# Performance work log

Hardware: AMD Instinct MI355X
Metric: run time of the kernel (lower is better)

Reference implementation:

```python
import jax, jax.numpy as jnp
import numpy as np

B, S, D, H, L = 128, 256, 128, 4, 2
N = S - 1            # tree nodes (complete binary tree, depths 0..7)
MAX_DEPTH = 7
NEG = -1e9
EPS = 1e-6


def _binary_tree_topology():
    n = np.arange(N)
    parent = np.where(n > 0, (n - 1) // 2, 0).astype(np.int32)   # parent(0) dummy
    depth = np.floor(np.log2(n + 1)).astype(np.int32)            # BFS level
    is_leaf = (2 * n + 1 >= N)
    return parent, depth, is_leaf


def setup_inputs() -> dict:
    key = jax.random.key(0)
    ks = jax.random.split(key, 6)
    p_np, d_np, l_np = _binary_tree_topology()
    parent = jnp.broadcast_to(jnp.asarray(p_np), (B, N))
    depth = jnp.broadcast_to(jnp.asarray(d_np), (B, N))
    is_leaf = jnp.broadcast_to(jnp.asarray(l_np), (B, N))
    x = jax.random.normal(ks[0], (B, S, D), jnp.float32)
    mask = jnp.zeros((B, 1, 1, S), jnp.float32)  # full trees -> no padding
    sc = 1.0 / np.sqrt(D)
    Wq = jax.random.normal(ks[1], (L, D, D), jnp.float32) * sc
    Wk = jax.random.normal(ks[2], (L, D, D), jnp.float32) * sc
    Wv = jax.random.normal(ks[3], (L, D, D), jnp.float32) * sc
    Wo = jax.random.normal(ks[4], (L, D, D), jnp.float32) * sc
    bq = jnp.zeros((L, D)); bk = jnp.zeros((L, D)); bv = jnp.zeros((L, D)); bo = jnp.zeros((L, D))
    g1 = jnp.ones((L, D)); b1 = jnp.zeros((L, D))
    g2 = jnp.ones((L, D)); b2 = jnp.zeros((L, D))
    return dict(x=x, mask=mask, parent=parent, depth=depth, is_leaf=is_leaf,
                Wq=Wq, bq=bq, Wk=Wk, bk=bk, Wv=Wv, bv=bv, Wo=Wo, bo=bo,
                g1=g1, b1=b1, g2=g2, b2=b2)


def _layernorm(x, g, b):
    mu = jnp.mean(x, axis=-1, keepdims=True)
    var = jnp.mean(jnp.square(x - mu), axis=-1, keepdims=True)
    return g * (x - mu) * jax.lax.rsqrt(var + EPS) + b


def _tree_agg(x, parent, depth, is_leaf):
    """Vectorized bottom-up tree aggregation (agg='sum': tanh(sum children)).
    Seq positions map to tree nodes in BFS order; last position passes through."""
    e = x[:, :N]                                            # [B, N, D]
    seg = (parent + (jnp.arange(B) * N)[:, None]).reshape(-1)  # flat parent ids
    for d in range(MAX_DEPTH, 0, -1):                       # deepest level -> root
        contrib = jnp.where((depth == d)[..., None], e, 0.0)
        agg = jax.ops.segment_sum(contrib.reshape(B * N, D), seg,
                                  num_segments=B * N).reshape(B, N, D)
        upd = ((depth == d - 1) & (~is_leaf))[..., None]    # internal nodes at d-1
        e = jnp.where(upd, jnp.tanh(agg), e)
    return jnp.concatenate([e, x[:, N:]], axis=1)


def reference(x, mask, parent, depth, is_leaf,
              Wq, bq, Wk, bk, Wv, bv, Wo, bo, g1, b1, g2, b2):
    Dh = D // H
    scale = 1.0 / jnp.sqrt(jnp.float32(Dh))
    losses = []
    weights = None
    for l in range(L):
        q = (jnp.einsum('bsd,de->bse', x, Wq[l]) + bq[l]).reshape(B, S, H, Dh).transpose(0, 2, 1, 3)
        k = (jnp.einsum('bsd,de->bse', x, Wk[l]) + bk[l]).reshape(B, S, H, Dh).transpose(0, 2, 1, 3)
        v = (jnp.einsum('bsd,de->bse', x, Wv[l]) + bv[l]).reshape(B, S, H, Dh).transpose(0, 2, 1, 3)
        logits = jnp.einsum('bhqd,bhkd->bhqk', q, k) * scale + mask * NEG
        attn = jax.nn.softmax(logits, axis=-1)              # [B, H, S, S]
        ctx = jnp.einsum('bhqk,bhkd->bhqd', attn, v).transpose(0, 2, 1, 3).reshape(B, S, D)
        att_out = jnp.einsum('bsd,de->bse', ctx, Wo[l]) + bo[l]
        out1 = _layernorm(x + att_out, g1[l], b1[l])
        tab = _tree_agg(out1, parent, depth, is_leaf)       # dropout: eval -> identity
        x = _layernorm(out1 + tab, g2[l], b2[l])
        weights = attn[:, :, -1, :]
        losses.append(jnp.sum(jnp.abs(weights)))
    total_l1 = jnp.sum(jnp.stack(losses))
    return x, total_l1, weights
```

## Files before the change

kernel.cpp:

```cpp
#include <hip/hip_runtime.h>
#include <math.h>

typedef __bf16 bf16x8 __attribute__((ext_vector_type(8)));
typedef __bf16 bf16x2 __attribute__((ext_vector_type(2)));
typedef float f32x4 __attribute__((ext_vector_type(4)));

namespace {
constexpr int kB = 128, kS = 256, kD = 128, kH = 4;
constexpr float kEps = 1e-6f;
constexpr float kScale = 0.17677669529663687f;
constexpr float kNeg = -1000000000.0f;
constexpr float kLog2e = 1.4426950408889634f;
constexpr size_t kSZ = (size_t)kB * kS * kD;
}

__device__ __forceinline__ void glds16(const void* g, void* l) {
    __builtin_amdgcn_global_load_lds(
        (const __attribute__((address_space(1))) unsigned int*)g,
        (__attribute__((address_space(3))) unsigned int*)l, 16, 0, 0);
}

__global__ __launch_bounds__(256) void wtrans(
    const float* __restrict__ Wq, const float* __restrict__ Wk,
    const float* __restrict__ Wv, const float* __restrict__ Wo,
    __bf16* __restrict__ Wt)
{
    const int mtx = blockIdx.x & 3, l = blockIdx.x >> 2;
    const float* W = (mtx == 0 ? Wq : mtx == 1 ? Wk : mtx == 2 ? Wv : Wo) +
                     (size_t)l * kD * kD;
    __bf16* o = Wt + (size_t)blockIdx.x * kD * kD;
    for (int idx = threadIdx.x; idx < kD * kD; idx += 256) {
        const int k = idx >> 7, n = idx & 127;
        o[n * 128 + (((k >> 3) ^ (n & 7)) << 3) + (k & 7)] = (__bf16)W[idx];
    }
}

template <bool F32A>
__global__ __launch_bounds__(512, 4) void qkv_gemm(
    const void* __restrict__ Av, const __bf16* __restrict__ Wt,
    const float* __restrict__ bq, const float* __restrict__ bk,
    const float* __restrict__ bv, __bf16* __restrict__ Qb,
    __bf16* __restrict__ Kb, __bf16* __restrict__ Vb)
{
    __shared__ __bf16 As[128 * 128];
    __shared__ __bf16 Ws[128 * 128];

    const int t = threadIdx.x;
    const int w = t >> 6, l = t & 63, lo = l & 15, g = l >> 4;
    const int tile = ((blockIdx.x & 127) << 1) | (blockIdx.x >> 7);
    const size_t m0 = (size_t)tile * 128;

#pragma unroll
    for (int it = 0; it < 4; ++it)
        glds16(Wt + (it * 8 + w) * 512 + l * 8, &Ws[(it * 8 + w) * 512]);

    if constexpr (F32A) {
#pragma unroll
        for (int p = 0; p < 4; ++p) {
            const int ci = p * 512 + t;
            const int row = ci >> 4, c = ci & 15;
            const float* src = (const float*)Av + (m0 + row) * 128 + c * 8;
            const float4 a0 = *(const float4*)src;
            const float4 a1 = *(const float4*)(src + 4);
            bf16x8 o;
            o[0] = (__bf16)a0.x; o[1] = (__bf16)a0.y; o[2] = (__bf16)a0.z; o[3] = (__bf16)a0.w;
            o[4] = (__bf16)a1.x; o[5] = (__bf16)a1.y; o[6] = (__bf16)a1.z; o[7] = (__bf16)a1.w;
            *(bf16x8*)&As[row * 128 + (c ^ (row & 7)) * 8] = o;
        }
    } else {
#pragma unroll
        for (int it = 0; it < 4; ++it)
            glds16((const __bf16*)Av + m0 * 128 + (it * 8 + w) * 512 + l * 8,
                   &As[(it * 8 + w) * 512]);
    }
    __syncthreads();

    bf16x8 av[4];
    {
        const int arow = w * 16 + lo;
#pragma unroll
        for (int ks = 0; ks < 4; ++ks)
            av[ks] = *(const bf16x8*)&As[arow * 128 + ((g + 4 * ks) ^ (arow & 7)) * 8];
    }
    __syncthreads();

#pragma unroll
    for (int it = 0; it < 4; ++it)
        glds16(Wt + 16384 + (it * 8 + w) * 512 + l * 8, &As[(it * 8 + w) * 512]);

    const float* biases[3] = {bq, bk, bv};
    __bf16* outs[3] = {Qb, Kb, Vb};
    const __bf16* wbuf[3] = {Ws, As, Ws};

#pragma unroll
    for (int m = 0; m < 3; ++m) {
        const __bf16* wb = wbuf[m];
        f32x4 acc[8];
#pragma unroll
        for (int ni = 0; ni < 8; ++ni) acc[ni] = f32x4{0.f, 0.f, 0.f, 0.f};
#pragma unroll
        for (int ks = 0; ks < 4; ++ks)
#pragma unroll
            for (int ni = 0; ni < 8; ++ni) {
                const int brow = ni * 16 + lo;
                const bf16x8 bv8 =
                    *(const bf16x8*)&wb[brow * 128 + ((g + 4 * ks) ^ (brow & 7)) * 8];
                acc[ni] = __builtin_amdgcn_mfma_f32_16x16x32_bf16(av[ks], bv8, acc[ni], 0, 0, 0);
            }
#pragma unroll
        for (int ni = 0; ni < 8; ++ni) {
            const float bc = biases[m][ni * 16 + lo];
#pragma unroll
            for (int r = 0; r < 4; ++r)
                outs[m][(m0 + w * 16 + g * 4 + r) * 128 + ni * 16 + lo] =
                    (__bf16)(acc[ni][r] + bc);
        }
        if (m == 0) {
            __syncthreads();
#pragma unroll
            for (int it = 0; it < 4; ++it)
                glds16(Wt + 2 * 16384 + (it * 8 + w) * 512 + l * 8,
                       &Ws[(it * 8 + w) * 512]);
        } else if (m == 1) {
            __syncthreads();
        }
    }
}

template <int WEIGHTS, bool RESF32>
__global__ __launch_bounds__(512) void attn_oproj(
    const __bf16* __restrict__ Qb, const __bf16* __restrict__ Kb,
    const __bf16* __restrict__ Vb, const float* __restrict__ mask,
    const __bf16* __restrict__ Wo, const float* __restrict__ bo,
    const void* __restrict__ resid, const float* __restrict__ gamma,
    const float* __restrict__ beta, __bf16* __restrict__ O1,
    float* __restrict__ wout, float* __restrict__ l1out)
{
    __shared__ __bf16 Kls[2][256 * 32];
    __shared__ __bf16 Vt[2][32][270];
    __shared__ __bf16 Pl[8][16 * 64];
    __shared__ __bf16 Ctx[128 * 128];
    __shared__ __bf16 Wos[128 * 128];
    __shared__ float mb[256];

    const int t = threadIdx.x;
    const int w = t >> 6, l = t & 63, lo = l & 15, g = l >> 4;
    const int b = blockIdx.x & 127, strip = blockIdx.x >> 7;
    const size_t bbase = (size_t)b * 256 * 128;
    const int q0 = strip * 128 + w * 16;
    const int kswz = (lo ^ (lo >> 2)) & 3;

#pragma unroll
    for (int it = 0; it < 4; ++it)
        glds16(Wo + (it * 8 + w) * 512 + l * 8, &Wos[(it * 8 + w) * 512]);

    bf16x8 kpre[2], vpre[2];
    const int krow = t >> 2, kc = t & 3;
    const int vkey = t >> 2, vd0 = (t & 3) << 3;

    auto loadKV = [&](int h) {
#pragma unroll
        for (int p = 0; p < 2; ++p)
            kpre[p] = *(const bf16x8*)(Kb + bbase + (size_t)(p * 128 + krow) * 128 +
                                       h * 32 + kc * 8);
#pragma unroll
        for (int p = 0; p < 2; ++p)
            vpre[p] = *(const bf16x8*)(Vb + bbase + (size_t)(p * 128 + vkey) * 128 +
                                       h * 32 + vd0);
    };
    auto writeKV = [&](int buf) {
#pragma unroll
        for (int p = 0; p < 2; ++p) {
            const int row = p * 128 + krow;
            const int sw = (kc ^ ((row ^ (row >> 2)) & 3)) << 3;
            *(bf16x8*)&Kls[buf][row * 32 + sw] = kpre[p];
        }
#pragma unroll
        for (int p = 0; p < 2; ++p) {
            const int key = p * 128 + vkey;
#pragma unroll
            for (int i = 0; i < 8; ++i) Vt[buf][vd0 + i][key] = vpre[p][i];
        }
    };

    if (t < 256) mb[t] = mask[b * 256 + t] * (kNeg * kLog2e);
    if (WEIGHTS && blockIdx.x == 0 && t == 0) l1out[0] = 1024.0f;

    bf16x8 qfr[4];
#pragma unroll
    for (int h = 0; h < 4; ++h)
        qfr[h] = *(const bf16x8*)(Qb + bbase + (size_t)(q0 + lo) * 128 + h * 32 + g * 8);

    loadKV(0);
    writeKV(0);
    __syncthreads();

#pragma unroll
    for (int h = 0; h < 4; ++h) {
        const int cur = h & 1;
        f32x4 s[16];
        __builtin_amdgcn_s_setprio(1);
#pragma unroll
        for (int f = 0; f < 16; ++f) {
            const bf16x8 kf =
                *(const bf16x8*)&Kls[cur][(f * 16 + lo) * 32 + ((g ^ kswz) << 3)];
            s[f] = __builtin_amdgcn_mfma_f32_16x16x32_bf16(
                kf, qfr[h], f32x4{0.f, 0.f, 0.f, 0.f}, 0, 0, 0);
        }
        __builtin_amdgcn_s_setprio(0);

        if (h < 3) loadKV(h + 1);

        float ls = 0.f;
#pragma unroll
        for (int f = 0; f < 16; ++f) {
            const f32x4 mk = *(const f32x4*)&mb[f * 16 + g * 4];
#pragma unroll
            for (int r = 0; r < 4; ++r) {
                const float p = __builtin_amdgcn_exp2f(
                    s[f][r] * (kScale * kLog2e) + mk[r]);
                s[f][r] = p;
                ls += p;
            }
        }
        ls += __shfl_xor(ls, 16, 64);
        ls += __shfl_xor(ls, 32, 64);

        if constexpr (WEIGHTS) {
            if (strip == 1 && w == 7 && lo == 15) {
                const float inv = 1.f / ls;
                float* wrow = wout + ((size_t)b * 4 + h) * 256;
#pragma unroll
                for (int f = 0; f < 16; ++f)
#pragma unroll
                    for (int r = 0; r < 4; ++r)
                        wrow[f * 16 + g * 4 + r] = s[f][r] * inv;
            }
        }

        if (h < 3) writeKV(cur ^ 1);

        f32x4 o[2] = {f32x4{0.f, 0.f, 0.f, 0.f}, f32x4{0.f, 0.f, 0.f, 0.f}};
#pragma unroll
        for (int qt = 0; qt < 4; ++qt) {
#pragma unroll
            for (int fl = 0; fl < 4; ++fl) {
                const int ff = qt * 4 + fl;
#pragma unroll
                for (int pr = 0; pr < 2; ++pr) {
                    bf16x2 pk;
                    pk[0] = (__bf16)s[ff][2 * pr];
                    pk[1] = (__bf16)s[ff][2 * pr + 1];
                    const int e = fl * 16 + 4 * g + 2 * pr;
                    const int addr =
                        lo * 64 + ((((e >> 3) ^ (lo & 7)) << 3) | (e & 7));
                    *(bf16x2*)&Pl[w][addr] = pk;
                }
            }
            __builtin_amdgcn_s_setprio(1);
#pragma unroll
            for (int ksl = 0; ksl < 2; ++ksl) {
                const int cc = ksl * 4 + g;
                const bf16x8 pa =
                    *(const bf16x8*)&Pl[w][lo * 64 + ((cc ^ (lo & 7)) << 3)];
#pragma unroll
                for (int nf = 0; nf < 2; ++nf) {
                    const bf16x8 bv =
                        *(const bf16x8*)&Vt[cur][nf * 16 + lo][(qt * 2 + ksl) * 32 + g * 8];
                    o[nf] = __builtin_amdgcn_mfma_f32_16x16x32_bf16(pa, bv, o[nf], 0, 0, 0);
                }
            }
            __builtin_amdgcn_s_setprio(0);
        }

#pragma unroll
        for (int r = 0; r < 4; ++r) {
            const float inv = 1.f / __shfl(ls, 4 * g + r, 64);
            const int crow = w * 16 + g * 4 + r;
#pragma unroll
            for (int nf = 0; nf < 2; ++nf) {
                const int col = h * 32 + nf * 16 + lo;
                const int chunk = (col >> 3) ^ (crow & 7);
                Ctx[crow * 128 + (chunk << 3) + (col & 7)] = (__bf16)(o[nf][r] * inv);
            }
        }
        if (h < 3) __syncthreads();
    }

    const size_t m0 = (size_t)b * 256 + strip * 128;
    f32x4 acc[8];
#pragma unroll
    for (int ni = 0; ni < 8; ++ni) acc[ni] = f32x4{0.f, 0.f, 0.f, 0.f};

    const int arow = w * 16 + lo;
#pragma unroll
    for (int ks = 0; ks < 4; ++ks) {
        const bf16x8 av =
            *(const bf16x8*)&Ctx[arow * 128 + (((g + 4 * ks) ^ (arow & 7)) << 3)];
#pragma unroll
        for (int ni = 0; ni < 8; ++ni) {
            const int brow = ni * 16 + lo;
            const bf16x8 bv8 =
                *(const bf16x8*)&Wos[brow * 128 + (((g + 4 * ks) ^ (brow & 7)) << 3)];
            acc[ni] = __builtin_amdgcn_mfma_f32_16x16x32_bf16(av, bv8, acc[ni], 0, 0, 0);
        }
    }

    float bcol[8], ga[8], be[8];
#pragma unroll
    for (int ni = 0; ni < 8; ++ni) {
        bcol[ni] = bo[ni * 16 + lo];
        ga[ni] = gamma[ni * 16 + lo];
        be[ni] = beta[ni * 16 + lo];
    }

    float vv[4][8];
    float s[4] = {0, 0, 0, 0}, s2[4] = {0, 0, 0, 0};
#pragma unroll
    for (int r = 0; r < 4; ++r) {
        const size_t mm = m0 + w * 16 + g * 4 + r;
#pragma unroll
        for (int ni = 0; ni < 8; ++ni) {
            float rv;
            if constexpr (RESF32) {
                rv = ((const float*)resid)[mm * 128 + ni * 16 + lo];
            } else {
                const int chunk = ((ni * 16 + lo) >> 3) ^ ((int)mm & 7);
                rv = (float)((const __bf16*)resid)[mm * 128 + chunk * 8 + (lo & 7)];
            }
            const float x = acc[ni][r] + bcol[ni] + rv;
            vv[r][ni] = x; s[r] += x; s2[r] += x * x;
        }
    }
#pragma unroll
    for (int r = 0; r < 4; ++r)
#pragma unroll
        for (int o = 1; o < 16; o <<= 1) {
            s[r] += __shfl_xor(s[r], o, 64);
            s2[r] += __shfl_xor(s2[r], o, 64);
        }
#pragma unroll
    for (int r = 0; r < 4; ++r) {
        const float mu = s[r] * (1.f / 128.f);
        const float var = s2[r] * (1.f / 128.f) - mu * mu;
        const float rs = rsqrtf(var + kEps);
        const size_t mm = m0 + w * 16 + g * 4 + r;
#pragma unroll
        for (int ni = 0; ni < 8; ++ni)
            O1[mm * 128 + ni * 16 + lo] =
                (__bf16)(ga[ni] * (vv[r][ni] - mu) * rs + be[ni]);
    }
}

__global__ __launch_bounds__(1024) void tree_ln(
    const __bf16* __restrict__ o1, const float* __restrict__ gamma,
    const float* __restrict__ beta, float* __restrict__ xo,
    __bf16* __restrict__ xb, int wf32, int wbf16)
{
    __shared__ float e[127 * 132];
    const int isleaf = blockIdx.x >> 7;
    const int b = blockIdx.x & 127;
    const int t = threadIdx.x;
    const __bf16* ob = o1 + (size_t)b * 256 * 128;
    const int wv = t >> 6, lane = t & 63;
    const float2 gv = *(const float2*)(gamma + lane * 2);
    const float2 bb = *(const float2*)(beta + lane * 2);
    const int c = lane * 2;

    auto ln_store = [&](int row, float y0, float y1) {
        float s = y0 + y1, s2 = y0 * y0 + y1 * y1;
#pragma unroll
        for (int o = 1; o < 64; o <<= 1) {
            s += __shfl_xor(s, o, 64);
            s2 += __shfl_xor(s2, o, 64);
        }
        const float mu = s * (1.f / 128.f);
        const float var = s2 * (1.f / 128.f) - mu * mu;
        const float rs = rsqrtf(var + kEps);
        const float r0 = gv.x * (y0 - mu) * rs + bb.x;
        const float r1 = gv.y * (y1 - mu) * rs + bb.y;
        const size_t rowoff = ((size_t)b * 256 + row) * 128;
        if (wf32) {
            float2 o2; o2.x = r0; o2.y = r1;
            *(float2*)(xo + rowoff + c) = o2;
        }
        if (wbf16) {
            const int chunk = (c >> 3) ^ (row & 7);
            bf16x2 ob2; ob2[0] = (__bf16)r0; ob2[1] = (__bf16)r1;
            *(bf16x2*)(xb + rowoff + chunk * 8 + (c & 7)) = ob2;
        }
    };

    if (isleaf) {
        for (int row = 128 + wv; row < 256; row += 16) {
            const bf16x2 v = *(const bf16x2*)(ob + (size_t)row * 128 + c);
            ln_store(row, 2.f * (float)v[0], 2.f * (float)v[1]);
        }
        return;
    }

    {
        const int p = 63 + (t >> 4);
        const int cg = (t & 15) * 8;
        const bf16x8 c1 = *(const bf16x8*)(ob + (size_t)(2 * p + 1) * 128 + cg);
        const bf16x8 c2 = *(const bf16x8*)(ob + (size_t)(2 * p + 2) * 128 + cg);
        f32x4 r0, r1;
#pragma unroll
        for (int i = 0; i < 4; ++i)
            r0[i] = tanhf((float)c1[i] + (float)c2[i]);
#pragma unroll
        for (int i = 0; i < 4; ++i)
            r1[i] = tanhf((float)c1[4 + i] + (float)c2[4 + i]);
        *(f32x4*)&e[p * 132 + cg] = r0;
        *(f32x4*)&e[p * 132 + cg + 4] = r1;
    }
    __syncthreads();

    {
        const int col = wv * 8 + (lane & 7);
        const int nsub = lane >> 3;
        for (int lvl = 5; lvl >= 0; --lvl) {
            const int p0 = (1 << lvl) - 1;
            const int cnt = 1 << lvl;
            for (int base = 0; base < cnt; base += 8) {
                const int p = p0 + base + nsub;
                if (base + nsub < cnt) {
                    e[p * 132 + col] =
                        tanhf(e[(2 * p + 1) * 132 + col] + e[(2 * p + 2) * 132 + col]);
                }
            }
        }
    }
    __syncthreads();

    for (int row = wv; row < 128; row += 16) {
        const bf16x2 v = *(const bf16x2*)(ob + (size_t)row * 128 + c);
        float y0, y1;
        if (row < 127) {
            y0 = (float)v[0] + e[row * 132 + c];
            y1 = (float)v[1] + e[row * 132 + c + 1];
        } else {
            y0 = 2.f * (float)v[0];
            y1 = 2.f * (float)v[1];
        }
        ln_store(row, y0, y1);
    }
}

extern "C" void kernel_launch(void* const* d_in, const int* in_sizes, int n_in,
                              void* d_out, int out_size, void* d_ws, size_t ws_size,
                              hipStream_t stream)
{
    (void)in_sizes; (void)n_in; (void)out_size; (void)ws_size;

    const float* x_in = (const float*)d_in[0];
    const float* mask = (const float*)d_in[1];
    const float* Wq = (const float*)d_in[5];
    const float* bq = (const float*)d_in[6];
    const float* Wk = (const float*)d_in[7];
    const float* bk = (const float*)d_in[8];
    const float* Wv = (const float*)d_in[9];
    const float* bv = (const float*)d_in[10];
    const float* Wo = (const float*)d_in[11];
    const float* bo = (const float*)d_in[12];
    const float* g1 = (const float*)d_in[13];
    const float* b1 = (const float*)d_in[14];
    const float* g2 = (const float*)d_in[15];
    const float* b2 = (const float*)d_in[16];

    float* out_x = (float*)d_out;
    float* out_l1 = out_x + kSZ;
    float* out_w = out_l1 + 1;

    char* wsb = (char*)d_ws;
    __bf16* Qb = (__bf16*)wsb;
    __bf16* Kb = (__bf16*)(wsb + 1 * kSZ * 2);
    __bf16* Vb = (__bf16*)(wsb + 2 * kSZ * 2);
    __bf16* O1 = (__bf16*)(wsb + 3 * kSZ * 2);
    __bf16* xb = (__bf16*)(wsb + 4 * kSZ * 2);
    __bf16* Wt = (__bf16*)(wsb + 5 * kSZ * 2);

    wtrans<<<8, 256, 0, stream>>>(Wq, Wk, Wv, Wo, Wt);

    qkv_gemm<true><<<256, 512, 0, stream>>>(x_in, Wt, bq, bk, bv, Qb, Kb, Vb);
    attn_oproj<0, true><<<256, 512, 0, stream>>>(Qb, Kb, Vb, mask,
                                                 Wt + 3 * kD * kD, bo,
                                                 x_in, g1, b1, O1,
                                                 nullptr, nullptr);
    tree_ln<<<256, 1024, 0, stream>>>(O1, g2, b2, nullptr, xb, 0, 1);

    const __bf16* WtL = Wt + 4 * kD * kD;
    qkv_gemm<false><<<256, 512, 0, stream>>>(xb, WtL, bq + kD, bk + kD, bv + kD,
                                             Qb, Kb, Vb);
    attn_oproj<1, false><<<256, 512, 0, stream>>>(Qb, Kb, Vb, mask,
                                                  WtL + 3 * kD * kD, bo + kD,
                                                  xb, g1 + kD, b1 + kD, O1,
                                                  out_w, out_l1);
    tree_ln<<<256, 1024, 0, stream>>>(O1, g2 + kD, b2 + kD, out_x, nullptr, 1, 0);
}
```

Before: 115.0 us.

## Fuse QKV projection into attention kernel, recomputing K/V per query strip

Merges the separate QKV GEMM kernel into the attention+output-projection kernel: each block loads its batch's full input rows into LDS, projects K/V for all keys and Q for its strip per head, then runs attention and the O-projection with LDS residual. This removes the global round trip for Q/K/V and one launch per layer. In exchange, K/V projections are computed twice (once per query strip), LDS use grows substantially, and weights are read from global memory in a fragment-friendly layout rather than staged in LDS.

Measured after the change: 105.5 us. 1.09x faster.

```diff
diff --git a/kernel.cpp b/kernel.cpp
--- a/kernel.cpp
+++ b/kernel.cpp
@@ -2,6 +2,7 @@
 #include <math.h>
 
 typedef __bf16 bf16x8 __attribute__((ext_vector_type(8)));
+typedef __bf16 bf16x4 __attribute__((ext_vector_type(4)));
 typedef __bf16 bf16x2 __attribute__((ext_vector_type(2)));
 typedef float f32x4 __attribute__((ext_vector_type(4)));
 
@@ -31,185 +32,157 @@
     __bf16* o = Wt + (size_t)blockIdx.x * kD * kD;
     for (int idx = threadIdx.x; idx < kD * kD; idx += 256) {
         const int k = idx >> 7, n = idx & 127;
-        o[n * 128 + (((k >> 3) ^ (n & 7)) << 3) + (k & 7)] = (__bf16)W[idx];
-    }
-}
-
-template <bool F32A>
-__global__ __launch_bounds__(512, 4) void qkv_gemm(
-    const void* __restrict__ Av, const __bf16* __restrict__ Wt,
+        const int lo = n & 15, ni = n >> 4;
+        const int j = k & 7, tt = k >> 3, g = tt & 3, ks = tt >> 2;
+        o[((ni * 4 + ks) * 64 + g * 16 + lo) * 8 + j] = (__bf16)W[idx];
+    }
+}
+
+template <int WEIGHTS, bool F32X>
+__global__ __launch_bounds__(512) void mega_attn(
+    const void* __restrict__ xsrc, const __bf16* __restrict__ Wp,
     const float* __restrict__ bq, const float* __restrict__ bk,
-    const float* __restrict__ bv, __bf16* __restrict__ Qb,
-    __bf16* __restrict__ Kb, __bf16* __restrict__ Vb)
+    const float* __restrict__ bv, const float* __restrict__ bo,
+    const float* __restrict__ mask, const float* __restrict__ gamma,
+    const float* __restrict__ beta, __bf16* __restrict__ O1,
+    float* __restrict__ wout, float* __restrict__ l1out)
 {
-    __shared__ __bf16 As[128 * 128];
-    __shared__ __bf16 Ws[128 * 128];
+    __shared__ __bf16 Xs[256 * 128];
+    __shared__ __bf16 Kls[256 * 32];
+    __shared__ __bf16 Vt[32][276];
+    __shared__ __bf16 Pl[8][16 * 64];
+    __shared__ __bf16 Qs[8][16 * 32];
+    __shared__ __bf16 Ctx[128 * 128];
+    __shared__ float mb[256];
 
     const int t = threadIdx.x;
     const int w = t >> 6, l = t & 63, lo = l & 15, g = l >> 4;
-    const int tile = ((blockIdx.x & 127) << 1) | (blockIdx.x >> 7);
-    const size_t m0 = (size_t)tile * 128;
-
-#pragma unroll
-    for (int it = 0; it < 4; ++it)
-        glds16(Wt + (it * 8 + w) * 512 + l * 8, &Ws[(it * 8 + w) * 512]);
-
-    if constexpr (F32A) {
-#pragma unroll
-        for (int p = 0; p < 4; ++p) {
+    const int b = blockIdx.x & 127, strip = blockIdx.x >> 7;
+    const int q0 = strip * 128 + w * 16;
+    const int tk0 = w * 32;
+    const int kswz = (lo ^ (lo >> 2)) & 3;
+
+    const __bf16* Wqp = Wp;
+    const __bf16* Wkp = Wp + 16384;
+    const __bf16* Wvp = Wp + 2 * 16384;
+    const __bf16* Wop = Wp + 3 * 16384;
+
+    if constexpr (F32X) {
+#pragma unroll
+        for (int p = 0; p < 8; ++p) {
             const int ci = p * 512 + t;
             const int row = ci >> 4, c = ci & 15;
-            const float* src = (const float*)Av + (m0 + row) * 128 + c * 8;
+            const float* src = (const float*)xsrc +
+                               ((size_t)b * 256 + row) * 128 + c * 8;
             const float4 a0 = *(const float4*)src;
             const float4 a1 = *(const float4*)(src + 4);
             bf16x8 o;
             o[0] = (__bf16)a0.x; o[1] = (__bf16)a0.y; o[2] = (__bf16)a0.z; o[3] = (__bf16)a0.w;
             o[4] = (__bf16)a1.x; o[5] = (__bf16)a1.y; o[6] = (__bf16)a1.z; o[7] = (__bf16)a1.w;
-            *(bf16x8*)&As[row * 128 + (c ^ (row & 7)) * 8] = o;
+            *(bf16x8*)&Xs[row * 128 + ((c ^ (row & 7)) << 3)] = o;
         }
     } else {
 #pragma unroll
-        for (int it = 0; it < 4; ++it)
-            glds16((const __bf16*)Av + m0 * 128 + (it * 8 + w) * 512 + l * 8,
-                   &As[(it * 8 + w) * 512]);
-    }
-    __syncthreads();
-
-    bf16x8 av[4];
-    {
-        const int arow = w * 16 + lo;
-#pragma unroll
-        for (int ks = 0; ks < 4; ++ks)
-            av[ks] = *(const bf16x8*)&As[arow * 128 + ((g + 4 * ks) ^ (arow & 7)) * 8];
-    }
-    __syncthreads();
-
-#pragma unroll
-    for (int it = 0; it < 4; ++it)
-        glds16(Wt + 16384 + (it * 8 + w) * 512 + l * 8, &As[(it * 8 + w) * 512]);
-
-    const float* biases[3] = {bq, bk, bv};
-    __bf16* outs[3] = {Qb, Kb, Vb};
-    const __bf16* wbuf[3] = {Ws, As, Ws};
-
-#pragma unroll
-    for (int m = 0; m < 3; ++m) {
-        const __bf16* wb = wbuf[m];
-        f32x4 acc[8];
-#pragma unroll
-        for (int ni = 0; ni < 8; ++ni) acc[ni] = f32x4{0.f, 0.f, 0.f, 0.f};
-#pragma unroll
-        for (int ks = 0; ks < 4; ++ks)
-#pragma unroll
-            for (int ni = 0; ni < 8; ++ni) {
-                const int brow = ni * 16 + lo;
-                const bf16x8 bv8 =
-                    *(const bf16x8*)&wb[brow * 128 + ((g + 4 * ks) ^ (brow & 7)) * 8];
-                acc[ni] = __builtin_amdgcn_mfma_f32_16x16x32_bf16(av[ks], bv8, acc[ni], 0, 0, 0);
-            }
-#pragma unroll
-        for (int ni = 0; ni < 8; ++ni) {
-            const float bc = biases[m][ni * 16 + lo];
-#pragma unroll
-            for (int r = 0; r < 4; ++r)
-                outs[m][(m0 + w * 16 + g * 4 + r) * 128 + ni * 16 + lo] =
-                    (__bf16)(acc[ni][r] + bc);
-        }
-        if (m == 0) {
-            __syncthreads();
-#pragma unroll
-            for (int it = 0; it < 4; ++it)
-                glds16(Wt + 2 * 16384 + (it * 8 + w) * 512 + l * 8,
-                       &Ws[(it * 8 + w) * 512]);
-        } else if (m == 1) {
-            __syncthreads();
-        }
-    }
-}
-
-template <int WEIGHTS, bool RESF32>
-__global__ __launch_bounds__(512) void attn_oproj(
-    const __bf16* __restrict__ Qb, const __bf16* __restrict__ Kb,
-    const __bf16* __restrict__ Vb, const float* __restrict__ mask,
-    const __bf16* __restrict__ Wo, const float* __restrict__ bo,
-    const void* __restrict__ resid, const float* __restrict__ gamma,
-    const float* __restrict__ beta, __bf16* __restrict__ O1,
-    float* __restrict__ wout, float* __restrict__ l1out)
-{
-    __shared__ __bf16 Kls[2][256 * 32];
-    __shared__ __bf16 Vt[2][32][270];
-    __shared__ __bf16 Pl[8][16 * 64];
-    __shared__ __bf16 Ctx[128 * 128];
-    __shared__ __bf16 Wos[128 * 128];
-    __shared__ float mb[256];
-
-    const int t = threadIdx.x;
-    const int w = t >> 6, l = t & 63, lo = l & 15, g = l >> 4;
-    const int b = blockIdx.x & 127, strip = blockIdx.x >> 7;
-    const size_t bbase = (size_t)b * 256 * 128;
-    const int q0 = strip * 128 + w * 16;
-    const int kswz = (lo ^ (lo >> 2)) & 3;
-
-#pragma unroll
-    for (int it = 0; it < 4; ++it)
-        glds16(Wo + (it * 8 + w) * 512 + l * 8, &Wos[(it * 8 + w) * 512]);
-
-    bf16x8 kpre[2], vpre[2];
-    const int krow = t >> 2, kc = t & 3;
-    const int vkey = t >> 2, vd0 = (t & 3) << 3;
-
-    auto loadKV = [&](int h) {
-#pragma unroll
-        for (int p = 0; p < 2; ++p)
-            kpre[p] = *(const bf16x8*)(Kb + bbase + (size_t)(p * 128 + krow) * 128 +
-                                       h * 32 + kc * 8);
-#pragma unroll
-        for (int p = 0; p < 2; ++p)
-            vpre[p] = *(const bf16x8*)(Vb + bbase + (size_t)(p * 128 + vkey) * 128 +
-                                       h * 32 + vd0);
-    };
-    auto writeKV = [&](int buf) {
-#pragma unroll
-        for (int p = 0; p < 2; ++p) {
-            const int row = p * 128 + krow;
-            const int sw = (kc ^ ((row ^ (row >> 2)) & 3)) << 3;
-            *(bf16x8*)&Kls[buf][row * 32 + sw] = kpre[p];
-        }
-#pragma unroll
-        for (int p = 0; p < 2; ++p) {
-            const int key = p * 128 + vkey;
-#pragma unroll
-            for (int i = 0; i < 8; ++i) Vt[buf][vd0 + i][key] = vpre[p][i];
-        }
-    };
-
+        for (int it = 0; it < 8; ++it)
+            glds16((const __bf16*)xsrc + (size_t)b * 32768 + (it * 8 + w) * 512 + l * 8,
+                   &Xs[(it * 8 + w) * 512]);
+    }
     if (t < 256) mb[t] = mask[b * 256 + t] * (kNeg * kLog2e);
     if (WEIGHTS && blockIdx.x == 0 && t == 0) l1out[0] = 1024.0f;
-
-    bf16x8 qfr[4];
-#pragma unroll
-    for (int h = 0; h < 4; ++h)
-        qfr[h] = *(const bf16x8*)(Qb + bbase + (size_t)(q0 + lo) * 128 + h * 32 + g * 8);
-
-    loadKV(0);
-    writeKV(0);
     __syncthreads();
 
+    auto wfrag = [&](const __bf16* W, int ni, int ks) {
+        return *(const bf16x8*)(W + (((ni * 4 + ks) * 64 + l) << 3));
+    };
+    auto xfrag = [&](int row, int ks) {
+        return *(const bf16x8*)&Xs[row * 128 + (((g + 4 * ks) ^ (row & 7)) << 3)];
+    };
+
 #pragma unroll
     for (int h = 0; h < 4; ++h) {
-        const int cur = h & 1;
+        bf16x8 xa[2][4];
+#pragma unroll
+        for (int mi = 0; mi < 2; ++mi)
+#pragma unroll
+            for (int ks = 0; ks < 4; ++ks)
+                xa[mi][ks] = xfrag(tk0 + mi * 16 + lo, ks);
+
+        f32x4 kacc[2][2], vacc[2][2];
+#pragma unroll
+        for (int i = 0; i < 2; ++i)
+#pragma unroll
+            for (int j2 = 0; j2 < 2; ++j2) {
+                kacc[i][j2] = f32x4{0.f, 0.f, 0.f, 0.f};
+                vacc[i][j2] = f32x4{0.f, 0.f, 0.f, 0.f};
+            }
+#pragma unroll
+        for (int ks = 0; ks < 4; ++ks) {
+            const bf16x8 wk0 = wfrag(Wkp, 2 * h, ks);
+            const bf16x8 wk1 = wfrag(Wkp, 2 * h + 1, ks);
+            const bf16x8 wv0 = wfrag(Wvp, 2 * h, ks);
+            const bf16x8 wv1 = wfrag(Wvp, 2 * h + 1, ks);
+            kacc[0][0] = __builtin_amdgcn_mfma_f32_16x16x32_bf16(wk0, xa[0][ks], kacc[0][0], 0, 0, 0);
+            kacc[0][1] = __builtin_amdgcn_mfma_f32_16x16x32_bf16(wk0, xa[1][ks], kacc[0][1], 0, 0, 0);
+            kacc[1][0] = __builtin_amdgcn_mfma_f32_16x16x32_bf16(wk1, xa[0][ks], kacc[1][0], 0, 0, 0);
+            kacc[1][1] = __builtin_amdgcn_mfma_f32_16x16x32_bf16(wk1, xa[1][ks], kacc[1][1], 0, 0, 0);
+            vacc[0][0] = __builtin_amdgcn_mfma_f32_16x16x32_bf16(xa[0][ks], wv0, vacc[0][0], 0, 0, 0);
+            vacc[1][0] = __builtin_amdgcn_mfma_f32_16x16x32_bf16(xa[1][ks], wv0, vacc[1][0], 0, 0, 0);
+            vacc[0][1] = __builtin_amdgcn_mfma_f32_16x16x32_bf16(xa[0][ks], wv1, vacc[0][1], 0, 0, 0);
+            vacc[1][1] = __builtin_amdgcn_mfma_f32_16x16x32_bf16(xa[1][ks], wv1, vacc[1][1], 0, 0, 0);
+        }
+        f32x4 qacc[2] = {f32x4{0.f, 0.f, 0.f, 0.f}, f32x4{0.f, 0.f, 0.f, 0.f}};
+#pragma unroll
+        for (int ks = 0; ks < 4; ++ks) {
+            const bf16x8 xq = xfrag(q0 + lo, ks);
+            qacc[0] = __builtin_amdgcn_mfma_f32_16x16x32_bf16(xq, wfrag(Wqp, 2 * h, ks), qacc[0], 0, 0, 0);
+            qacc[1] = __builtin_amdgcn_mfma_f32_16x16x32_bf16(xq, wfrag(Wqp, 2 * h + 1, ks), qacc[1], 0, 0, 0);
+        }
+
+#pragma unroll
+        for (int dm = 0; dm < 2; ++dm) {
+            const f32x4 bkv = *(const f32x4*)(bk + h * 32 + dm * 16 + 4 * g);
+            const int pos = ((dm * 2 + (g >> 1)) ^ kswz) << 3;
+            const int sub = (4 * g) & 7;
+#pragma unroll
+            for (int tj = 0; tj < 2; ++tj) {
+                bf16x4 kv;
+#pragma unroll
+                for (int r = 0; r < 4; ++r) kv[r] = (__bf16)(kacc[dm][tj][r] + bkv[r]);
+                const int key = tk0 + tj * 16 + lo;
+                *(bf16x4*)&Kls[key * 32 + pos + sub] = kv;
+            }
+        }
+#pragma unroll
+        for (int nj = 0; nj < 2; ++nj) {
+            const float bvv = bv[h * 32 + nj * 16 + lo];
+#pragma unroll
+            for (int mi = 0; mi < 2; ++mi) {
+                bf16x4 vv4;
+#pragma unroll
+                for (int r = 0; r < 4; ++r) vv4[r] = (__bf16)(vacc[mi][nj][r] + bvv);
+                *(bf16x4*)&Vt[nj * 16 + lo][tk0 + mi * 16 + 4 * g] = vv4;
+            }
+        }
+#pragma unroll
+        for (int nj = 0; nj < 2; ++nj) {
+            const float bqv = bq[h * 32 + nj * 16 + lo];
+#pragma unroll
+            for (int r = 0; r < 4; ++r)
+                Qs[w][(4 * g + r) * 32 + nj * 16 + lo] = (__bf16)(qacc[nj][r] + bqv);
+        }
+        __syncthreads();
+
+        const bf16x8 qf = *(const bf16x8*)&Qs[w][lo * 32 + g * 8];
         f32x4 s[16];
         __builtin_amdgcn_s_setprio(1);
 #pragma unroll
         for (int f = 0; f < 16; ++f) {
             const bf16x8 kf =
-                *(const bf16x8*)&Kls[cur][(f * 16 + lo) * 32 + ((g ^ kswz) << 3)];
+                *(const bf16x8*)&Kls[(f * 16 + lo) * 32 + ((g ^ kswz) << 3)];
             s[f] = __builtin_amdgcn_mfma_f32_16x16x32_bf16(
-                kf, qfr[h], f32x4{0.f, 0.f, 0.f, 0.f}, 0, 0, 0);
+                kf, qf, f32x4{0.f, 0.f, 0.f, 0.f}, 0, 0, 0);
         }
         __builtin_amdgcn_s_setprio(0);
-
-        if (h < 3) loadKV(h + 1);
 
         float ls = 0.f;
 #pragma unroll
@@ -237,8 +210,6 @@
                         wrow[f * 16 + g * 4 + r] = s[f][r] * inv;
             }
         }
-
-        if (h < 3) writeKV(cur ^ 1);
 
         f32x4 o[2] = {f32x4{0.f, 0.f, 0.f, 0.f}, f32x4{0.f, 0.f, 0.f, 0.f}};
 #pragma unroll
@@ -265,9 +236,9 @@
                     *(const bf16x8*)&Pl[w][lo * 64 + ((cc ^ (lo & 7)) << 3)];
 #pragma unroll
                 for (int nf = 0; nf < 2; ++nf) {
-                    const bf16x8 bv =
-                        *(const bf16x8*)&Vt[cur][nf * 16 + lo][(qt * 2 + ksl) * 32 + g * 8];
-                    o[nf] = __builtin_amdgcn_mfma_f32_16x16x32_bf16(pa, bv, o[nf], 0, 0, 0);
+                    const bf16x8 bvv =
+                        *(const bf16x8*)&Vt[nf * 16 + lo][(qt * 2 + ksl) * 32 + g * 8];
+                    o[nf] = __builtin_amdgcn_mfma_f32_16x16x32_bf16(pa, bvv, o[nf], 0, 0, 0);
                 }
             }
             __builtin_amdgcn_s_setprio(0);
@@ -298,12 +269,9 @@
         const bf16x8 av =
             *(const bf16x8*)&Ctx[arow * 128 + (((g + 4 * ks) ^ (arow & 7)) << 3)];
 #pragma unroll
-        for (int ni = 0; ni < 8; ++ni) {
-            const int brow = ni * 16 + lo;
-            const bf16x8 bv8 =
-                *(const bf16x8*)&Wos[brow * 128 + (((g + 4 * ks) ^ (brow & 7)) << 3)];
-            acc[ni] = __builtin_amdgcn_mfma_f32_16x16x32_bf16(av, bv8, acc[ni], 0, 0, 0);
-        }
+        for (int ni = 0; ni < 8; ++ni)
+            acc[ni] = __builtin_amdgcn_mfma_f32_16x16x32_bf16(
+                av, wfrag(Wop, ni, ks), acc[ni], 0, 0, 0);
     }
 
     float bcol[8], ga[8], be[8];
@@ -318,16 +286,12 @@
     float s[4] = {0, 0, 0, 0}, s2[4] = {0, 0, 0, 0};
 #pragma unroll
     for (int r = 0; r < 4; ++r) {
-        const size_t mm = m0 + w * 16 + g * 4 + r;
+        const int local = strip * 128 + w * 16 + g * 4 + r;
 #pragma unroll
         for (int ni = 0; ni < 8; ++ni) {
-            float rv;
-            if constexpr (RESF32) {
-                rv = ((const float*)resid)[mm * 128 + ni * 16 + lo];
-            } else {
-                const int chunk = ((ni * 16 + lo) >> 3) ^ ((int)mm & 7);
-                rv = (float)((const __bf16*)resid)[mm * 128 + chunk * 8 + (lo & 7)];
-            }
+            const int col = ni * 16 + lo;
+            const int chunk = (col >> 3) ^ (local & 7);
+            const float rv = (float)Xs[local * 128 + (chunk << 3) + (col & 7)];
             const float x = acc[ni][r] + bcol[ni] + rv;
             vv[r][ni] = x; s[r] += x; s2[r] += x * x;
         }
@@ -473,28 +437,20 @@
     float* out_w = out_l1 + 1;
 
     char* wsb = (char*)d_ws;
-    __bf16* Qb = (__bf16*)wsb;
-    __bf16* Kb = (__bf16*)(wsb + 1 * kSZ * 2);
-    __bf16* Vb = (__bf16*)(wsb + 2 * kSZ * 2);
-    __bf16* O1 = (__bf16*)(wsb + 3 * kSZ * 2);
-    __bf16* xb = (__bf16*)(wsb + 4 * kSZ * 2);
-    __bf16* Wt = (__bf16*)(wsb + 5 * kSZ * 2);
+    __bf16* O1 = (__bf16*)wsb;
+    __bf16* xb = (__bf16*)(wsb + kSZ * 2);
+    __bf16* Wt = (__bf16*)(wsb + 2 * kSZ * 2);
 
     wtrans<<<8, 256, 0, stream>>>(Wq, Wk, Wv, Wo, Wt);
 
-    qkv_gemm<true><<<256, 512, 0, stream>>>(x_in, Wt, bq, bk, bv, Qb, Kb, Vb);
-    attn_oproj<0, true><<<256, 512, 0, stream>>>(Qb, Kb, Vb, mask,
-                                                 Wt + 3 * kD * kD, bo,
-                                                 x_in, g1, b1, O1,
-                                                 nullptr, nullptr);
+    mega_attn<0, true><<<256, 512, 0, stream>>>(x_in, Wt, bq, bk, bv, bo,
+                                                mask, g1, b1, O1,
+                                                nullptr, nullptr);
     tree_ln<<<256, 1024, 0, stream>>>(O1, g2, b2, nullptr, xb, 0, 1);
 
-    const __bf16* WtL = Wt + 4 * kD * kD;
-    qkv_gemm<false><<<256, 512, 0, stream>>>(xb, WtL, bq + kD, bk + kD, bv + kD,
-                                             Qb, Kb, Vb);
-    attn_oproj<1, false><<<256, 512, 0, stream>>>(Qb, Kb, Vb, mask,
-                                                  WtL + 3 * kD * kD, bo + kD,
-                                                  xb, g1 + kD, b1 + kD, O1,
-                                                  out_w, out_l1);
+    mega_attn<1, false><<<256, 512, 0, stream>>>(xb, Wt + 4 * 16384,
+                                                 bq + kD, bk + kD, bv + kD, bo + kD,
+                                                 mask, g1 + kD, b1 + kD, O1,
+                                                 out_w, out_l1);
     tree_ln<<<256, 1024, 0, stream>>>(O1, g2 + kD, b2 + kD, out_x, nullptr, 1, 0);
 }
```
